# Kernel optimization log

Hardware: AMD Instinct MI355X
Metric: run time of the kernel (lower is better)

Reference implementation:

```python
import jax, jax.numpy as jnp
import numpy as np

HIDDEN = 1024
HEADS = 16
HEAD_DIM = HIDDEN // HEADS  # 64
B, S = 2, 2048


def setup_inputs() -> dict:
    key = jax.random.key(0)
    ks = jax.random.split(key, 8)
    scale = 1.0 / np.sqrt(HIDDEN)
    return {
        "hidden_states": jax.random.normal(ks[0], (B, S, HIDDEN), dtype=jnp.float32),
        "head_mask": jnp.ones((1, HEADS, 1, 1), dtype=jnp.float32),
        "Wq": jax.random.normal(ks[1], (HIDDEN, HIDDEN), dtype=jnp.float32) * scale,
        "bq": jnp.zeros((HIDDEN,), dtype=jnp.float32),
        "Wk": jax.random.normal(ks[2], (HIDDEN, HIDDEN), dtype=jnp.float32) * scale,
        "bk": jnp.zeros((HIDDEN,), dtype=jnp.float32),
        "Wv": jax.random.normal(ks[3], (HIDDEN, HIDDEN), dtype=jnp.float32) * scale,
        "bv": jnp.zeros((HIDDEN,), dtype=jnp.float32),
    }


def _split_heads(x):
    # [B, S, HIDDEN] -> [B, HEADS, S, HEAD_DIM]
    b, s, _ = x.shape
    return x.reshape(b, s, HEADS, HEAD_DIM).transpose(0, 2, 1, 3)


def reference(hidden_states, head_mask, Wq, bq, Wk, bk, Wv, bv):
    q = _split_heads(hidden_states @ Wq + bq)
    k = _split_heads(hidden_states @ Wk + bk)
    v = _split_heads(hidden_states @ Wv + bv)
    # [B, H, S, S] attention scores (eager, full matrix as in original)
    scores = jnp.einsum("bhqd,bhkd->bhqk", q, k) / jnp.sqrt(jnp.float32(HEAD_DIM))
    probs = jax.nn.softmax(scores, axis=-1)
    probs = probs * head_mask  # post-softmax multiplicative head mask
    ctx = jnp.einsum("bhqk,bhkd->bhqd", probs, v)
    b, h, s, d = ctx.shape
    return ctx.transpose(0, 2, 1, 3).reshape(b, s, h * d)
```

## Files before the change

### kernel.cpp

```cpp
#include <hip/hip_runtime.h>
#include <hip/hip_bf16.h>
#include <stdint.h>

#define B_  2
#define S_  2048
#define H_  16
#define D_  64
#define HID 1024

typedef __bf16 bf16x8 __attribute__((ext_vector_type(8)));
typedef float  f32x4  __attribute__((ext_vector_type(4)));
typedef float  f32x16 __attribute__((ext_vector_type(16)));
typedef unsigned int u32x4 __attribute__((ext_vector_type(4)));
typedef unsigned short ush;

__device__ __forceinline__ ush f2bf(float f) {
    __bf16 b = (__bf16)f;
    return __builtin_bit_cast(ush, b);
}
__device__ __forceinline__ unsigned pk2(float a, float b) {
    return (unsigned)f2bf(a) | ((unsigned)f2bf(b) << 16);
}
__device__ __forceinline__ float xchg32f(float x) {
    return __shfl_xor(x, 32, 64);
}
__device__ __forceinline__ float exp2fast(float x) {
#if __has_builtin(__builtin_amdgcn_exp2f)
    return __builtin_amdgcn_exp2f(x);
#else
    float r; asm("v_exp_f32 %0, %1" : "=v"(r) : "v"(x)); return r;
#endif
}
__device__ __forceinline__ void gld16(const void* g, void* l) {
    __builtin_amdgcn_global_load_lds(
        (const __attribute__((address_space(1))) unsigned*)g,
        (__attribute__((address_space(3))) unsigned*)l, 16, 0, 0);
}
#define MFMA32(a, b, c) __builtin_amdgcn_mfma_f32_32x32x16_bf16(a, b, c, 0, 0, 0)

__global__ __launch_bounds__(256) void cvt_hid(const float* __restrict__ in,
                                               ush* __restrict__ outp) {
    size_t base = ((size_t)blockIdx.x * 256 + threadIdx.x) * 16;
    #pragma unroll
    for (int half = 0; half < 2; ++half) {
        float4 v0 = *reinterpret_cast<const float4*>(in + base + half * 8);
        float4 v1 = *reinterpret_cast<const float4*>(in + base + half * 8 + 4);
        u32x4 o = { pk2(v0.x, v0.y), pk2(v0.z, v0.w),
                    pk2(v1.x, v1.y), pk2(v1.z, v1.w) };
        *reinterpret_cast<u32x4*>(outp + base + half * 8) = o;
    }
}

__global__ __launch_bounds__(256) void wtrans(
    const float* __restrict__ Wq, const float* __restrict__ Wk,
    const float* __restrict__ Wv, ush* __restrict__ wt)
{
    const int tid = threadIdx.x;
    const int k0 = blockIdx.x * 64, n0 = blockIdx.y * 64, sel = blockIdx.z;
    const float* W = sel == 0 ? Wq : (sel == 1 ? Wk : Wv);
    ush* o = wt + (size_t)sel * HID * HID;
    __shared__ ush lT[64][72];
    #pragma unroll
    for (int i = 0; i < 4; ++i) {
        int c = tid + i * 256;
        int kr = c >> 4, c4 = (c & 15) << 2;
        float4 v = *reinterpret_cast<const float4*>(W + (size_t)(k0 + kr) * HID + n0 + c4);
        lT[kr][c4 + 0] = f2bf(v.x); lT[kr][c4 + 1] = f2bf(v.y);
        lT[kr][c4 + 2] = f2bf(v.z); lT[kr][c4 + 3] = f2bf(v.w);
    }
    __syncthreads();
    #pragma unroll
    for (int i = 0; i < 2; ++i) {
        int c = tid + i * 256;
        int nr = c >> 3, k8 = (c & 7) << 3;
        ush t[8];
        #pragma unroll
        for (int u = 0; u < 8; ++u) t[u] = lT[k8 + u][nr];
        u32x4 ov = { (unsigned)t[0] | ((unsigned)t[1] << 16),
                     (unsigned)t[2] | ((unsigned)t[3] << 16),
                     (unsigned)t[4] | ((unsigned)t[5] << 16),
                     (unsigned)t[6] | ((unsigned)t[7] << 16) };
        *reinterpret_cast<u32x4*>(o + (size_t)(n0 + nr) * HID + k0 + k8) = ov;
    }
}

__global__ __launch_bounds__(256) void proj(
    const ush* __restrict__ hidb, const ush* __restrict__ wt,
    const float* __restrict__ bq, const float* __restrict__ bk,
    const float* __restrict__ bv,
    ush* __restrict__ qd, ush* __restrict__ kd, ush* __restrict__ vtd)
{
    const int tid = threadIdx.x;
    const int wave = tid >> 6, lane = tid & 63;
    const int fr = lane & 15, fq = lane >> 4;
    const int wr = wave >> 1, wc = wave & 1;
    const int m0 = blockIdx.x * 128;
    const int n0 = blockIdx.y * 128;
    const int wsel = n0 >> 10;

    __shared__ char pool[65536];

    const int cr = lane >> 3;
    const int cs = lane & 7;

    f32x4 acc[4][4] = {};

    const ush* Asrc = hidb + (size_t)m0 * HID;
    const ush* Bsrc = wt + (size_t)n0 * HID;

    auto stage = [&](int buf, int kk) {
        #pragma unroll
        for (int j = 0; j < 4; ++j) {
            int ch = wave * 4 + j;
            int r = ch * 8 + cr;
            int so = kk + ((cs ^ (r & 7)) << 3);
            gld16(Asrc + (size_t)r * HID + so, pool + buf * 16384 + ch * 1024);
            gld16(Bsrc + (size_t)r * HID + so, pool + 32768 + buf * 16384 + ch * 1024);
        }
    };

    stage(0, 0);
    __syncthreads();
    int buf = 0;
    for (int ks = 0; ks < 16; ++ks) {
        if (ks < 15) stage(buf ^ 1, (ks + 1) * 64);
        const char* ab = pool + buf * 16384;
        const char* bb = pool + 32768 + buf * 16384;
        #pragma unroll
        for (int c = 0; c < 2; ++c) {
            bf16x8 a[4], b[4];
            #pragma unroll
            for (int i = 0; i < 4; ++i) {
                int ra = wr * 64 + i * 16 + fr;
                a[i] = *reinterpret_cast<const bf16x8*>(
                    ab + ((ra * 128 + c * 64 + fq * 16) ^ ((ra & 7) << 4)));
                int rb = wc * 64 + i * 16 + fr;
                b[i] = *reinterpret_cast<const bf16x8*>(
                    bb + ((rb * 128 + c * 64 + fq * 16) ^ ((rb & 7) << 4)));
            }
            __builtin_amdgcn_s_setprio(1);
            #pragma unroll
            for (int i = 0; i < 4; ++i)
                #pragma unroll
                for (int j = 0; j < 4; ++j)
                    acc[i][j] = __builtin_amdgcn_mfma_f32_16x16x32_bf16(
                        a[i], b[j], acc[i][j], 0, 0, 0);
            __builtin_amdgcn_s_setprio(0);
        }
        __syncthreads();
        buf ^= 1;
    }

    const int bi = m0 >> 11;
    const int s0 = m0 & 2047;
    const float* bias = wsel == 0 ? bq : (wsel == 1 ? bk : bv);
    const int nb = n0 & 1023;

    if (wsel < 2) {
        ush* dst = wsel == 0 ? qd : kd;
        const float scale = wsel == 0 ? 0.18033688011112042f : 1.0f;
        #pragma unroll
        for (int j = 0; j < 4; ++j) {
            int n = nb + wc * 64 + j * 16 + fr;
            int hh = n >> 6, d = n & 63;
            float bb2 = bias[n];
            const size_t rowb = (size_t)(bi * H_ + hh) * S_;
            #pragma unroll
            for (int i = 0; i < 4; ++i)
                #pragma unroll
                for (int e = 0; e < 4; ++e) {
                    int s = s0 + wr * 64 + i * 16 + fq * 4 + e;
                    dst[(rowb + s) * D_ + d] = f2bf((acc[i][j][e] + bb2) * scale);
                }
        }
    } else {
        ush (*lT)[136] = (ush (*)[136])pool;
        #pragma unroll
        for (int j = 0; j < 4; ++j) {
            int nl = wc * 64 + j * 16 + fr;
            float bb2 = bias[nb + nl];
            #pragma unroll
            for (int i = 0; i < 4; ++i)
                #pragma unroll
                for (int e = 0; e < 4; ++e)
                    lT[wr * 64 + i * 16 + fq * 4 + e][nl] = f2bf(acc[i][j][e] + bb2);
        }
        __syncthreads();
        #pragma unroll
        for (int c2 = 0; c2 < 8; ++c2) {
            int cid = tid + c2 * 256;
            int nl = cid >> 4, s8 = (cid & 15) * 8;
            int n = nb + nl, hh = n >> 6, d = n & 63;
            ush t[8];
            #pragma unroll
            for (int u = 0; u < 8; ++u) t[u] = lT[s8 + u][nl];
            u32x4 ov = { (unsigned)t[0] | ((unsigned)t[1] << 16),
                         (unsigned)t[2] | ((unsigned)t[3] << 16),
                         (unsigned)t[4] | ((unsigned)t[5] << 16),
                         (unsigned)t[6] | ((unsigned)t[7] << 16) };
            *reinterpret_cast<u32x4*>(
                vtd + ((size_t)(bi * H_ + hh) * D_ + d) * S_ + s0 + s8) = ov;
        }
    }
}

#define STAGE(sb, kv0) do {                                                    \
    gld16(K + (size_t)((kv0) + kr) * D_ + ss,      pool + (sb) * 16384 + wave * 1024); \
    gld16(K + (size_t)((kv0) + 64 + kr) * D_ + ss, pool + (sb) * 16384 + 8192 + wave * 1024); \
    gld16(VT + (size_t)dr * S_ + (kv0) + ss,       pool + 32768 + (sb) * 16384 + wave * 1024); \
    gld16(VT + (size_t)dr * S_ + (kv0) + 64 + ss,  pool + 32768 + (sb) * 16384 + 8192 + wave * 1024); \
} while (0)

#define WAITV0() asm volatile("s_waitcnt vmcnt(0)" ::: "memory")
#define BARRIER() do { __builtin_amdgcn_s_barrier();                           \
                       __builtin_amdgcn_sched_barrier(0); } while (0)

#define EXPPACK(pp0, pp1, ssum, pf) do {                                       \
    float t0 = 0.f, t1 = 0.f, t2 = 0.f, t3 = 0.f;                              \
    _Pragma("unroll")                                                          \
    for (int r = 0; r < 16; r += 4) {                                          \
        pp0[r]     = exp2fast(pp0[r]);     t0 += pp0[r];                       \
        pp0[r + 1] = exp2fast(pp0[r + 1]); t1 += pp0[r + 1];                   \
        pp0[r + 2] = exp2fast(pp0[r + 2]); t2 += pp0[r + 2];                   \
        pp0[r + 3] = exp2fast(pp0[r + 3]); t3 += pp0[r + 3];                   \
        pp1[r]     = exp2fast(pp1[r]);     t0 += pp1[r];                       \
        pp1[r + 1] = exp2fast(pp1[r + 1]); t1 += pp1[r + 1];                   \
        pp1[r + 2] = exp2fast(pp1[r + 2]); t2 += pp1[r + 2];                   \
        pp1[r + 3] = exp2fast(pp1[r + 3]); t3 += pp1[r + 3];                   \
    }                                                                          \
    ssum += (t0 + t1) + (t2 + t3);                                             \
    pf[0] = u32x4{pk2(pp0[0], pp0[1]),  pk2(pp0[2], pp0[3]),                   \
                  pk2(pp0[4], pp0[5]),  pk2(pp0[6], pp0[7])};                  \
    pf[1] = u32x4{pk2(pp0[8], pp0[9]),  pk2(pp0[10], pp0[11]),                 \
                  pk2(pp0[12], pp0[13]),pk2(pp0[14], pp0[15])};                \
    pf[2] = u32x4{pk2(pp1[0], pp1[1]),  pk2(pp1[2], pp1[3]),                   \
                  pk2(pp1[4], pp1[5]),  pk2(pp1[6], pp1[7])};                  \
    pf[3] = u32x4{pk2(pp1[8], pp1[9]),  pk2(pp1[10], pp1[11]),                 \
                  pk2(pp1[12], pp1[13]),pk2(pp1[14], pp1[15])};                \
} while (0)

__global__ __launch_bounds__(512) void attn(
    const ush* __restrict__ qg, const ush* __restrict__ kg,
    const ush* __restrict__ vtg, const float* __restrict__ hm,
    float* __restrict__ out)
{
    const int tid = threadIdx.x;
    const int wave = tid >> 6, lane = tid & 63;
    const int l31 = lane & 31, hi = lane >> 5;
    const int swz = (l31 & 7) << 4;
    const int g = blockIdx.x & 31, qt = blockIdx.x >> 5;
    const int h = g >> 1, bi = g & 1;
    const int qsub = wave & 3, par = wave >> 2;
    const size_t ho = (size_t)(bi * H_ + h) * S_ * D_;
    const ush* Q  = qg + ho;
    const ush* K  = kg + ho;
    const ush* VT = vtg + ho;

    __shared__ __align__(16) char pool[67584];

    const int dr = wave * 8 + (lane >> 3);
    const int kr = (dr & ~12) | ((dr & 4) << 1) | ((dr & 8) >> 1);
    const int ss = ((lane & 7) ^ (lane >> 3)) * 8;

    const int q0 = qt * 256 + qsub * 64 + l31;
    bf16x8 qfA[4], qfB[4];
    #pragma unroll
    for (int ks = 0; ks < 4; ++ks) {
        qfA[ks] = *reinterpret_cast<const bf16x8*>(Q + (size_t)q0 * D_ + ks * 16 + hi * 8);
        qfB[ks] = *reinterpret_cast<const bf16x8*>(Q + (size_t)(q0 + 32) * D_ + ks * 16 + hi * 8);
    }

    f32x16 aA0 = {}, aA1 = {}, aB0 = {}, aB1 = {};
    float sA = 0.f, sB = 0.f;

    STAGE(0, 0);
    WAITV0(); BARRIER();

    for (int s = 0; s < 16; ++s) {
        if (s < 15) STAGE((s + 1) & 1, (s + 1) * 128);
        const char* kb = pool + (s & 1) * 16384 + par * 8192;
        const char* vb = pool + 32768 + (s & 1) * 16384 + par * 8192;

        f32x16 p0A = {}, p1A = {}, p0B = {}, p1B = {};
        #pragma unroll
        for (int ks = 0; ks < 4; ++ks) {
            const int o = l31 * 128 + ks * 32 + hi * 16;
            bf16x8 k0 = *reinterpret_cast<const bf16x8*>(kb + (o ^ swz));
            bf16x8 k1 = *reinterpret_cast<const bf16x8*>(kb + ((o + 4096) ^ swz));
            __builtin_amdgcn_s_setprio(1);
            p0A = MFMA32(k0, qfA[ks], p0A);
            p1A = MFMA32(k1, qfA[ks], p1A);
            p0B = MFMA32(k0, qfB[ks], p0B);
            p1B = MFMA32(k1, qfB[ks], p1B);
            __builtin_amdgcn_s_setprio(0);
        }

        u32x4 pfA[4], pfB[4];
        EXPPACK(p0A, p1A, sA, pfA);
        EXPPACK(p0B, p1B, sB, pfB);

        #pragma unroll
        for (int ksc = 0; ksc < 4; ++ksc) {
            const int o = l31 * 128 + ksc * 32 + hi * 16;
            bf16x8 v0 = *reinterpret_cast<const bf16x8*>(vb + (o ^ swz));
            bf16x8 v1 = *reinterpret_cast<const bf16x8*>(vb + ((o + 4096) ^ swz));
            bf16x8 fA = __builtin_bit_cast(bf16x8, pfA[ksc]);
            bf16x8 fB = __builtin_bit_cast(bf16x8, pfB[ksc]);
            __builtin_amdgcn_s_setprio(1);
            aA0 = MFMA32(v0, fA, aA0);
            aA1 = MFMA32(v1, fA, aA1);
            aB0 = MFMA32(v0, fB, aB0);
            aB1 = MFMA32(v1, fB, aB1);
            __builtin_amdgcn_s_setprio(0);
        }

        WAITV0(); BARRIER();
    }

    sA += xchg32f(sA);
    sB += xchg32f(sB);
    float* cbase = (float*)pool;
    float* lbase = (float*)(pool + 65536);

    if (par == 1) {
        #pragma unroll
        for (int c = 0; c < 4; ++c) {
            *(f32x4*)(cbase + qsub * 4096 + (0 * 4 + c) * 256 + lane * 4) =
                f32x4{aA0[c * 4], aA0[c * 4 + 1], aA0[c * 4 + 2], aA0[c * 4 + 3]};
            *(f32x4*)(cbase + qsub * 4096 + (1 * 4 + c) * 256 + lane * 4) =
                f32x4{aA1[c * 4], aA1[c * 4 + 1], aA1[c * 4 + 2], aA1[c * 4 + 3]};
            *(f32x4*)(cbase + qsub * 4096 + (2 * 4 + c) * 256 + lane * 4) =
                f32x4{aB0[c * 4], aB0[c * 4 + 1], aB0[c * 4 + 2], aB0[c * 4 + 3]};
            *(f32x4*)(cbase + qsub * 4096 + (3 * 4 + c) * 256 + lane * 4) =
                f32x4{aB1[c * 4], aB1[c * 4 + 1], aB1[c * 4 + 2], aB1[c * 4 + 3]};
        }
        lbase[qsub * 128 + lane * 2]     = sA;
        lbase[qsub * 128 + lane * 2 + 1] = sB;
    }
    __syncthreads();
    if (par == 0) {
        #pragma unroll
        for (int c = 0; c < 4; ++c) {
            f32x4 t;
            t = *(const f32x4*)(cbase + qsub * 4096 + (0 * 4 + c) * 256 + lane * 4);
            aA0[c*4] += t[0]; aA0[c*4+1] += t[1]; aA0[c*4+2] += t[2]; aA0[c*4+3] += t[3];
            t = *(const f32x4*)(cbase + qsub * 4096 + (1 * 4 + c) * 256 + lane * 4);
            aA1[c*4] += t[0]; aA1[c*4+1] += t[1]; aA1[c*4+2] += t[2]; aA1[c*4+3] += t[3];
            t = *(const f32x4*)(cbase + qsub * 4096 + (2 * 4 + c) * 256 + lane * 4);
            aB0[c*4] += t[0]; aB0[c*4+1] += t[1]; aB0[c*4+2] += t[2]; aB0[c*4+3] += t[3];
            t = *(const f32x4*)(cbase + qsub * 4096 + (3 * 4 + c) * 256 + lane * 4);
            aB1[c*4] += t[0]; aB1[c*4+1] += t[1]; aB1[c*4+2] += t[2]; aB1[c*4+3] += t[3];
        }
        const float liA = sA + lbase[qsub * 128 + lane * 2];
        const float liB = sB + lbase[qsub * 128 + lane * 2 + 1];
        const float hmv = hm[h];
        const float invA = hmv / liA, invB = hmv / liB;
        float* orA = out + ((size_t)bi * S_ + q0) * HID + h * D_;
        float* orB = out + ((size_t)bi * S_ + q0 + 32) * HID + h * D_;
        #pragma unroll
        for (int gg = 0; gg < 4; ++gg) {
            f32x4 o0, o1, o2, o3;
            #pragma unroll
            for (int e = 0; e < 4; ++e) {
                o0[e] = aA0[gg * 4 + e] * invA;
                o1[e] = aA1[gg * 4 + e] * invA;
                o2[e] = aB0[gg * 4 + e] * invB;
                o3[e] = aB1[gg * 4 + e] * invB;
            }
            *reinterpret_cast<f32x4*>(orA + gg * 8 + hi * 4)      = o0;
            *reinterpret_cast<f32x4*>(orA + 32 + gg * 8 + hi * 4) = o1;
            *reinterpret_cast<f32x4*>(orB + gg * 8 + hi * 4)      = o2;
            *reinterpret_cast<f32x4*>(orB + 32 + gg * 8 + hi * 4) = o3;
        }
    }
}

extern "C" void kernel_launch(void* const* d_in, const int* in_sizes, int n_in,
                              void* d_out, int out_size, void* d_ws, size_t ws_size,
                              hipStream_t stream) {
    const float* hid = (const float*)d_in[0];
    const float* hm  = (const float*)d_in[1];
    const float* Wq  = (const float*)d_in[2];
    const float* bq  = (const float*)d_in[3];
    const float* Wk  = (const float*)d_in[4];
    const float* bk  = (const float*)d_in[5];
    const float* Wv  = (const float*)d_in[6];
    const float* bv  = (const float*)d_in[7];
    float* out = (float*)d_out;

    const size_t NE = (size_t)B_ * H_ * S_ * D_;
    ush* qws  = (ush*)d_ws;
    ush* kws  = qws + NE;
    ush* vt   = kws + NE;
    ush* hidb = (ush*)d_out;
    ush* wt   = hidb + NE;

    cvt_hid<<<1024, 256, 0, stream>>>(hid, hidb);
    wtrans<<<dim3(16, 16, 3), 256, 0, stream>>>(Wq, Wk, Wv, wt);
    proj<<<dim3(32, 24), 256, 0, stream>>>(hidb, wt, bq, bk, bv, qws, kws, vt);
    attn<<<256, 512, 0, stream>>>(qws, kws, vt, hm, out);
}
```

Measured before the change: 89.63 us.

## Software-pipeline attention loop with 4-stage LDS ring and interleaved exp/PV

Replaces the double-buffered KV loop with a fully unrolled four-buffer ring that keeps two tile loads in flight (partial vmcnt waits). It also software-pipelines the softmax: the exp/pack for tile t is interleaved chunk-by-chunk with the PV MFMAs of tile t-1, so the exp work can hide behind matrix ops. This doubles LDS use to about 130KB per block, which limits occupancy to one block per CU, and increases register pressure from the extra packed-probability buffers.

After: 199.5 us. +122.6%, slower.

```diff
diff --git a/kernel.cpp b/kernel.cpp
--- a/kernel.cpp
+++ b/kernel.cpp
@@ -204,39 +204,87 @@
     }
 }
 
-#define STAGE(sb, kv0) do {                                                    \
-    gld16(K + (size_t)((kv0) + kr) * D_ + ss,      pool + (sb) * 16384 + wave * 1024); \
-    gld16(K + (size_t)((kv0) + 64 + kr) * D_ + ss, pool + (sb) * 16384 + 8192 + wave * 1024); \
-    gld16(VT + (size_t)dr * S_ + (kv0) + ss,       pool + 32768 + (sb) * 16384 + wave * 1024); \
-    gld16(VT + (size_t)dr * S_ + (kv0) + 64 + ss,  pool + 32768 + (sb) * 16384 + 8192 + wave * 1024); \
-} while (0)
-
+#define WAITV4() asm volatile("s_waitcnt vmcnt(4)" ::: "memory")
 #define WAITV0() asm volatile("s_waitcnt vmcnt(0)" ::: "memory")
 #define BARRIER() do { __builtin_amdgcn_s_barrier();                           \
                        __builtin_amdgcn_sched_barrier(0); } while (0)
 
-#define EXPPACK(pp0, pp1, ssum, pf) do {                                       \
-    float t0 = 0.f, t1 = 0.f, t2 = 0.f, t3 = 0.f;                              \
+#define STAGE(b, t) do {                                                       \
+    const int kv0_ = (t) * 128;                                                \
+    char* Kb_ = pool + (b) * 32768;                                            \
+    char* Vb_ = Kb_ + 16384;                                                   \
+    gld16(K + (size_t)(kv0_ + kr) * D_ + ss,      Kb_ + wave * 1024);          \
+    gld16(K + (size_t)(kv0_ + 64 + kr) * D_ + ss, Kb_ + 8192 + wave * 1024);   \
+    gld16(VT + (size_t)dr * S_ + kv0_ + ss,       Vb_ + wave * 1024);          \
+    gld16(VT + (size_t)dr * S_ + kv0_ + 64 + ss,  Vb_ + 8192 + wave * 1024);   \
+} while (0)
+
+#define QKS(b) do {                                                            \
+    const char* kb_ = pool + (b) * 32768 + par * 8192;                         \
+    p0A = f32x16{}; p1A = f32x16{}; p0B = f32x16{}; p1B = f32x16{};            \
     _Pragma("unroll")                                                          \
-    for (int r = 0; r < 16; r += 4) {                                          \
-        pp0[r]     = exp2fast(pp0[r]);     t0 += pp0[r];                       \
-        pp0[r + 1] = exp2fast(pp0[r + 1]); t1 += pp0[r + 1];                   \
-        pp0[r + 2] = exp2fast(pp0[r + 2]); t2 += pp0[r + 2];                   \
-        pp0[r + 3] = exp2fast(pp0[r + 3]); t3 += pp0[r + 3];                   \
-        pp1[r]     = exp2fast(pp1[r]);     t0 += pp1[r];                       \
-        pp1[r + 1] = exp2fast(pp1[r + 1]); t1 += pp1[r + 1];                   \
-        pp1[r + 2] = exp2fast(pp1[r + 2]); t2 += pp1[r + 2];                   \
-        pp1[r + 3] = exp2fast(pp1[r + 3]); t3 += pp1[r + 3];                   \
+    for (int ks = 0; ks < 4; ++ks) {                                           \
+        const int o_ = l31 * 128 + ks * 32 + hi * 16;                          \
+        bf16x8 k0_ = *(const bf16x8*)(kb_ + (o_ ^ swz));                       \
+        bf16x8 k1_ = *(const bf16x8*)(kb_ + ((o_ + 4096) ^ swz));              \
+        __builtin_amdgcn_s_setprio(1);                                         \
+        p0A = MFMA32(k0_, qfA[ks], p0A); p1A = MFMA32(k1_, qfA[ks], p1A);      \
+        p0B = MFMA32(k0_, qfB[ks], p0B); p1B = MFMA32(k1_, qfB[ks], p1B);      \
+        __builtin_amdgcn_s_setprio(0);                                         \
     }                                                                          \
-    ssum += (t0 + t1) + (t2 + t3);                                             \
-    pf[0] = u32x4{pk2(pp0[0], pp0[1]),  pk2(pp0[2], pp0[3]),                   \
-                  pk2(pp0[4], pp0[5]),  pk2(pp0[6], pp0[7])};                  \
-    pf[1] = u32x4{pk2(pp0[8], pp0[9]),  pk2(pp0[10], pp0[11]),                 \
-                  pk2(pp0[12], pp0[13]),pk2(pp0[14], pp0[15])};                \
-    pf[2] = u32x4{pk2(pp1[0], pp1[1]),  pk2(pp1[2], pp1[3]),                   \
-                  pk2(pp1[4], pp1[5]),  pk2(pp1[6], pp1[7])};                  \
-    pf[3] = u32x4{pk2(pp1[8], pp1[9]),  pk2(pp1[10], pp1[11]),                 \
-                  pk2(pp1[12], pp1[13]),pk2(pp1[14], pp1[15])};                \
+} while (0)
+
+#define CHUNK_PV(vb, pfpA, pfpB, ksc) do {                                     \
+    const int o_ = l31 * 128 + (ksc) * 32 + hi * 16;                           \
+    bf16x8 v0_ = *(const bf16x8*)((vb) + (o_ ^ swz));                          \
+    bf16x8 v1_ = *(const bf16x8*)((vb) + ((o_ + 4096) ^ swz));                 \
+    bf16x8 fA_ = __builtin_bit_cast(bf16x8, pfpA[ksc]);                        \
+    bf16x8 fB_ = __builtin_bit_cast(bf16x8, pfpB[ksc]);                        \
+    __builtin_amdgcn_s_setprio(1);                                             \
+    aA0 = MFMA32(v0_, fA_, aA0); aA1 = MFMA32(v1_, fA_, aA1);                  \
+    aB0 = MFMA32(v0_, fB_, aB0); aB1 = MFMA32(v1_, fB_, aB1);                  \
+    __builtin_amdgcn_s_setprio(0);                                             \
+} while (0)
+
+#define CHUNK_EXP(pfcA, pfcB, ksc, pA, pB, hb) do {                            \
+    float a0_ = exp2fast(pA[(hb)+0]), a1_ = exp2fast(pA[(hb)+1]);              \
+    float a2_ = exp2fast(pA[(hb)+2]), a3_ = exp2fast(pA[(hb)+3]);              \
+    float a4_ = exp2fast(pA[(hb)+4]), a5_ = exp2fast(pA[(hb)+5]);              \
+    float a6_ = exp2fast(pA[(hb)+6]), a7_ = exp2fast(pA[(hb)+7]);              \
+    sA += ((a0_+a1_)+(a2_+a3_)) + ((a4_+a5_)+(a6_+a7_));                       \
+    pfcA[ksc] = u32x4{pk2(a0_,a1_), pk2(a2_,a3_), pk2(a4_,a5_), pk2(a6_,a7_)}; \
+    float b0_ = exp2fast(pB[(hb)+0]), b1_ = exp2fast(pB[(hb)+1]);              \
+    float b2_ = exp2fast(pB[(hb)+2]), b3_ = exp2fast(pB[(hb)+3]);              \
+    float b4_ = exp2fast(pB[(hb)+4]), b5_ = exp2fast(pB[(hb)+5]);              \
+    float b6_ = exp2fast(pB[(hb)+6]), b7_ = exp2fast(pB[(hb)+7]);              \
+    sB += ((b0_+b1_)+(b2_+b3_)) + ((b4_+b5_)+(b6_+b7_));                       \
+    pfcB[ksc] = u32x4{pk2(b0_,b1_), pk2(b2_,b3_), pk2(b4_,b5_), pk2(b6_,b7_)}; \
+} while (0)
+
+#define EXPPV(pfcA, pfcB, pfpA, pfpB, vbi) do {                                \
+    const char* vbp_ = pool + (vbi) * 32768 + 16384 + par * 8192;              \
+    CHUNK_PV(vbp_, pfpA, pfpB, 0); CHUNK_EXP(pfcA, pfcB, 0, p0A, p0B, 0);      \
+    CHUNK_PV(vbp_, pfpA, pfpB, 1); CHUNK_EXP(pfcA, pfcB, 1, p0A, p0B, 8);      \
+    CHUNK_PV(vbp_, pfpA, pfpB, 2); CHUNK_EXP(pfcA, pfcB, 2, p1A, p1B, 0);      \
+    CHUNK_PV(vbp_, pfpA, pfpB, 3); CHUNK_EXP(pfcA, pfcB, 3, p1A, p1B, 8);      \
+} while (0)
+
+#define EXPONLY(pfcA, pfcB) do {                                               \
+    CHUNK_EXP(pfcA, pfcB, 0, p0A, p0B, 0); CHUNK_EXP(pfcA, pfcB, 1, p0A, p0B, 8); \
+    CHUNK_EXP(pfcA, pfcB, 2, p1A, p1B, 0); CHUNK_EXP(pfcA, pfcB, 3, p1A, p1B, 8); \
+} while (0)
+
+#define PVONLY(pfpA, pfpB, vbi) do {                                           \
+    const char* vbp_ = pool + (vbi) * 32768 + 16384 + par * 8192;              \
+    CHUNK_PV(vbp_, pfpA, pfpB, 0); CHUNK_PV(vbp_, pfpA, pfpB, 1);              \
+    CHUNK_PV(vbp_, pfpA, pfpB, 2); CHUNK_PV(vbp_, pfpA, pfpB, 3);              \
+} while (0)
+
+#define ITER(t, bK, bS, bVp, pfcA, pfcB, pfpA, pfpB) do {                      \
+    WAITV4(); BARRIER();                                                       \
+    STAGE(bS, (t) + 2);                                                        \
+    QKS(bK);                                                                   \
+    EXPPV(pfcA, pfcB, pfpA, pfpB, bVp);                                        \
 } while (0)
 
 __global__ __launch_bounds__(512) void attn(
@@ -256,7 +304,7 @@
     const ush* K  = kg + ho;
     const ush* VT = vtg + ho;
 
-    __shared__ __align__(16) char pool[67584];
+    __shared__ __align__(16) char pool[133120];
 
     const int dr = wave * 8 + (lane >> 3);
     const int kr = (dr & ~12) | ((dr & 4) << 1) | ((dr & 8) >> 1);
@@ -271,56 +319,43 @@
     }
 
     f32x16 aA0 = {}, aA1 = {}, aB0 = {}, aB1 = {};
+    f32x16 p0A, p1A, p0B, p1B;
+    u32x4 pfEA[4], pfEB[4], pfOA[4], pfOB[4];
     float sA = 0.f, sB = 0.f;
 
-    STAGE(0, 0);
+    STAGE(0, 0); STAGE(1, 1);
+    WAITV4(); BARRIER();
+    STAGE(2, 2);
+    QKS(0);
+    EXPONLY(pfEA, pfEB);
+    WAITV4(); BARRIER();
+    STAGE(3, 3);
+    QKS(1);
+    EXPPV(pfOA, pfOB, pfEA, pfEB, 0);
+    ITER( 2, 2, 0, 1, pfEA, pfEB, pfOA, pfOB);
+    ITER( 3, 3, 1, 2, pfOA, pfOB, pfEA, pfEB);
+    ITER( 4, 0, 2, 3, pfEA, pfEB, pfOA, pfOB);
+    ITER( 5, 1, 3, 0, pfOA, pfOB, pfEA, pfEB);
+    ITER( 6, 2, 0, 1, pfEA, pfEB, pfOA, pfOB);
+    ITER( 7, 3, 1, 2, pfOA, pfOB, pfEA, pfEB);
+    ITER( 8, 0, 2, 3, pfEA, pfEB, pfOA, pfOB);
+    ITER( 9, 1, 3, 0, pfOA, pfOB, pfEA, pfEB);
+    ITER(10, 2, 0, 1, pfEA, pfEB, pfOA, pfOB);
+    ITER(11, 3, 1, 2, pfOA, pfOB, pfEA, pfEB);
+    ITER(12, 0, 2, 3, pfEA, pfEB, pfOA, pfOB);
+    ITER(13, 1, 3, 0, pfOA, pfOB, pfEA, pfEB);
+    WAITV4(); BARRIER();
+    QKS(2);
+    EXPPV(pfEA, pfEB, pfOA, pfOB, 1);
     WAITV0(); BARRIER();
-
-    for (int s = 0; s < 16; ++s) {
-        if (s < 15) STAGE((s + 1) & 1, (s + 1) * 128);
-        const char* kb = pool + (s & 1) * 16384 + par * 8192;
-        const char* vb = pool + 32768 + (s & 1) * 16384 + par * 8192;
-
-        f32x16 p0A = {}, p1A = {}, p0B = {}, p1B = {};
-        #pragma unroll
-        for (int ks = 0; ks < 4; ++ks) {
-            const int o = l31 * 128 + ks * 32 + hi * 16;
-            bf16x8 k0 = *reinterpret_cast<const bf16x8*>(kb + (o ^ swz));
-            bf16x8 k1 = *reinterpret_cast<const bf16x8*>(kb + ((o + 4096) ^ swz));
-            __builtin_amdgcn_s_setprio(1);
-            p0A = MFMA32(k0, qfA[ks], p0A);
-            p1A = MFMA32(k1, qfA[ks], p1A);
-            p0B = MFMA32(k0, qfB[ks], p0B);
-            p1B = MFMA32(k1, qfB[ks], p1B);
-            __builtin_amdgcn_s_setprio(0);
-        }
-
-        u32x4 pfA[4], pfB[4];
-        EXPPACK(p0A, p1A, sA, pfA);
-        EXPPACK(p0B, p1B, sB, pfB);
-
-        #pragma unroll
-        for (int ksc = 0; ksc < 4; ++ksc) {
-            const int o = l31 * 128 + ksc * 32 + hi * 16;
-            bf16x8 v0 = *reinterpret_cast<const bf16x8*>(vb + (o ^ swz));
-            bf16x8 v1 = *reinterpret_cast<const bf16x8*>(vb + ((o + 4096) ^ swz));
-            bf16x8 fA = __builtin_bit_cast(bf16x8, pfA[ksc]);
-            bf16x8 fB = __builtin_bit_cast(bf16x8, pfB[ksc]);
-            __builtin_amdgcn_s_setprio(1);
-            aA0 = MFMA32(v0, fA, aA0);
-            aA1 = MFMA32(v1, fA, aA1);
-            aB0 = MFMA32(v0, fB, aB0);
-            aB1 = MFMA32(v1, fB, aB1);
-            __builtin_amdgcn_s_setprio(0);
-        }
-
-        WAITV0(); BARRIER();
-    }
+    QKS(3);
+    EXPPV(pfOA, pfOB, pfEA, pfEB, 2);
+    PVONLY(pfOA, pfOB, 3);
 
     sA += xchg32f(sA);
     sB += xchg32f(sB);
     float* cbase = (float*)pool;
-    float* lbase = (float*)(pool + 65536);
+    float* lbase = (float*)(pool + 131072);
 
     if (par == 1) {
         #pragma unroll
```
